# Performance work log

Hardware: AMD Instinct MI355X
Metric: run time of the kernel (lower is better)

The kernel has to match this reference:

```python
import math
import jax, jax.numpy as jnp
import numpy as np

N_GAUSS = 1_000_000
EPS = 1e-8


def setup_inputs() -> dict:
    key = jax.random.key(0)
    k1, k2, k3 = jax.random.split(key, 3)
    init_extent = 50.0
    means = (jax.random.uniform(k1, (N_GAUSS, 3), dtype=jnp.float32) - 0.5) * 2.0 * init_extent
    log_scales = jnp.full((N_GAUSS, 3), math.log(0.05), dtype=jnp.float32)
    quats = jax.random.normal(k2, (N_GAUSS, 4), dtype=jnp.float32)
    sh_coeffs = jax.random.normal(k3, (N_GAUSS, 16, 3), dtype=jnp.float32) * 0.01
    opa_logit = math.log(0.1 / 0.9)  # inverse_sigmoid(init_opacity=0.1)
    opacity_camera = jnp.full((N_GAUSS, 1), opa_logit, dtype=jnp.float32)
    opacity_lidar = jnp.full((N_GAUSS, 1), opa_logit, dtype=jnp.float32)
    camera_to_world = jnp.eye(4, dtype=jnp.float32)
    lidar_to_world = jnp.eye(4, dtype=jnp.float32)
    intrinsics = jnp.array([[1000.0, 0.0, 800.0], [0.0, 1000.0, 450.0], [0.0, 0.0, 1.0]], dtype=jnp.float32)
    return dict(means=means, log_scales=log_scales, quats=quats, sh_coeffs=sh_coeffs,
                opacity_camera=opacity_camera, opacity_lidar=opacity_lidar,
                camera_to_world=camera_to_world, intrinsics=intrinsics,
                lidar_to_world=lidar_to_world,
                rgb_width=1600, rgb_height=900, lidar_width=1024, lidar_height=128,
                fov_min_deg=-25, fov_max_deg=3, near_plane=1, far_plane=100)


def _bilinear_scatter(u, v, w, vals, H, W, wrap_u):
    """Scatter vals [N,C] with weights w [N] at continuous pixel coords (u,v)
    using bilinear splatting. Returns [H, W, C+1] (weighted vals, weight sum)."""
    u0 = jnp.floor(u)
    v0 = jnp.floor(v)
    fu = u - u0
    fv = v - v0
    u0i = u0.astype(jnp.int32)
    v0i = v0.astype(jnp.int32)
    acc = jnp.zeros((H * W, vals.shape[-1] + 1), dtype=vals.dtype)
    corners = ((0, 0, (1.0 - fu) * (1.0 - fv)), (1, 0, fu * (1.0 - fv)),
               (0, 1, (1.0 - fu) * fv), (1, 1, fu * fv))
    for du, dv, cw in corners:
        ui = u0i + du
        vi = v0i + dv
        if wrap_u:
            ui = jnp.mod(ui, W)
            ok_u = jnp.ones_like(ui, dtype=bool)
        else:
            ok_u = (ui >= 0) & (ui < W)
        ok = ok_u & (vi >= 0) & (vi < H)
        ww = w * cw * ok.astype(w.dtype)
        idx = jnp.clip(vi, 0, H - 1) * W + jnp.clip(ui, 0, W - 1)
        payload = jnp.concatenate([vals * ww[:, None], ww[:, None]], axis=-1)
        acc = acc.at[idx].add(payload)
    return acc.reshape(H, W, -1)


def reference(means, log_scales, quats, sh_coeffs, opacity_camera, opacity_lidar,
              camera_to_world, intrinsics, lidar_to_world,
              rgb_width, rgb_height, lidar_width, lidar_height,
              fov_min_deg, fov_max_deg, near_plane, far_plane):
    H, W = int(rgb_height), int(rgb_width)
    HL, WL = int(lidar_height), int(lidar_width)
    near = float(near_plane)
    far = float(far_plane)

    # ---- camera (point-splat proxy of gsplat rasterization) ----
    w2c = jnp.linalg.inv(camera_to_world)
    pts_c = means @ w2c[:3, :3].T + w2c[:3, 3]  # [N,3] camera frame
    x, y, z = pts_c[:, 0], pts_c[:, 1], pts_c[:, 2]
    valid_c = (z > near) & (z < far)
    zs = jnp.where(valid_c, z, 1.0)
    u = intrinsics[0, 0] * x / zs + intrinsics[0, 2]
    v = intrinsics[1, 1] * y / zs + intrinsics[1, 2]
    opa_c = jax.nn.sigmoid(jnp.clip(opacity_camera[:, 0], -20.0, 20.0))
    colors = jax.nn.sigmoid(sh_coeffs[:, 0, :])  # DC band, as in render_rgb
    wc = opa_c * valid_c.astype(opa_c.dtype)
    vals_c = jnp.concatenate([colors, z[:, None]], axis=-1)  # [N,4] (rgb, depth)
    acc = _bilinear_scatter(u, v, wc, vals_c, H, W, wrap_u=False)
    wsum = acc[..., 4]
    alpha = jnp.clip(wsum, 0.0, 1.0)
    rgb = acc[..., :3] / (wsum[..., None] + EPS) * alpha[..., None]  # black background
    depth = acc[..., 3] / (wsum + EPS)

    # ---- LiDAR (custom spherical bilinear range-image splat, mean aggregation) ----
    w2l = jnp.linalg.inv(lidar_to_world)
    pts_l = means @ w2l[:3, :3].T + w2l[:3, 3]
    r = jnp.linalg.norm(pts_l, axis=-1)
    az = jnp.arctan2(pts_l[:, 1], pts_l[:, 0])
    el = jnp.arcsin(pts_l[:, 2] / jnp.maximum(r, 1e-6))
    fmin = math.radians(float(fov_min_deg))
    fmax = math.radians(float(fov_max_deg))
    uL = (az / (2.0 * jnp.pi) + 0.5) * WL          # azimuth wraps around
    vL = (fmax - el) / (fmax - fmin) * (HL - 1)    # elevation row
    valid_l = (r > near) & (r < far) & (el >= fmin) & (el <= fmax)
    opa_l = jax.nn.sigmoid(jnp.clip(opacity_lidar[:, 0], -20.0, 20.0))
    wl = opa_l * valid_l.astype(opa_l.dtype)
    acc_l = _bilinear_scatter(uL, vL, wl, r[:, None], HL, WL, wrap_u=True)
    lw = acc_l[..., 1]
    lidar_depth = acc_l[..., 0] / (lw + EPS)  # 'mean' depth aggregation
    lidar_alpha = jnp.clip(lw, 0.0, 1.0)

    return (rgb, depth, alpha, lidar_depth, lidar_alpha)
```

## Files before the change

### kernel.cpp

```cpp
#include <hip/hip_runtime.h>
#include <math.h>

#define EPSV 1e-8f
#define PI_D 3.14159265358979323846

__device__ float g_mats[32];

__device__ __forceinline__ void invert4x4_reg(const float* __restrict__ m,
                                              float* __restrict__ out) {
    double a00=m[0], a01=m[1], a02=m[2], a03=m[3];
    double a10=m[4], a11=m[5], a12=m[6], a13=m[7];
    double a20=m[8], a21=m[9], a22=m[10],a23=m[11];
    double a30=m[12],a31=m[13],a32=m[14],a33=m[15];

    double b00 = a00*a11 - a01*a10;
    double b01 = a00*a12 - a02*a10;
    double b02 = a00*a13 - a03*a10;
    double b03 = a01*a12 - a02*a11;
    double b04 = a01*a13 - a03*a11;
    double b05 = a02*a13 - a03*a12;
    double b06 = a20*a31 - a21*a30;
    double b07 = a20*a32 - a22*a30;
    double b08 = a20*a33 - a23*a30;
    double b09 = a21*a32 - a22*a31;
    double b10 = a21*a33 - a23*a31;
    double b11 = a22*a33 - a23*a32;

    double det = b00*b11 - b01*b10 + b02*b09 + b03*b08 - b04*b07 + b05*b06;
    double inv = 1.0 / det;

    out[0]  = (float)(( a11*b11 - a12*b10 + a13*b09) * inv);
    out[1]  = (float)((-a01*b11 + a02*b10 - a03*b09) * inv);
    out[2]  = (float)(( a31*b05 - a32*b04 + a33*b03) * inv);
    out[3]  = (float)((-a21*b05 + a22*b04 - a23*b03) * inv);
    out[4]  = (float)((-a10*b11 + a12*b08 - a13*b07) * inv);
    out[5]  = (float)(( a00*b11 - a02*b08 + a03*b07) * inv);
    out[6]  = (float)((-a30*b05 + a32*b02 - a33*b01) * inv);
    out[7]  = (float)(( a20*b05 - a22*b02 + a23*b01) * inv);
    out[8]  = (float)(( a10*b10 - a11*b08 + a13*b06) * inv);
    out[9]  = (float)((-a00*b10 + a01*b08 - a03*b06) * inv);
    out[10] = (float)(( a30*b04 - a31*b02 + a33*b00) * inv);
    out[11] = (float)((-a20*b04 + a21*b02 - a23*b00) * inv);
    out[12] = (float)((-a10*b09 + a11*b07 - a12*b06) * inv);
    out[13] = (float)(( a00*b09 - a01*b07 + a02*b06) * inv);
    out[14] = (float)((-a30*b03 + a31*b01 - a32*b00) * inv);
    out[15] = (float)(( a20*b03 - a21*b01 + a22*b00) * inv);
}

__global__ void prep_kernel(const float* __restrict__ c2w,
                            const float* __restrict__ l2w) {
    if (blockIdx.x == 0 && threadIdx.x == 0) {
        invert4x4_reg(c2w, g_mats);
        invert4x4_reg(l2w, g_mats + 16);
    }
}

__device__ __forceinline__ float sigmoid_clipped(float x) {
    #pragma clang fp contract(off)
    x = fminf(fmaxf(x, -20.0f), 20.0f);
    return 1.0f / (1.0f + expf(-x));
}

template<int MODE>
__global__ __launch_bounds__(256) void scatter_acc(
    const float* __restrict__ means,
    const float* __restrict__ sh,
    const float* __restrict__ opa_c,
    const float* __restrict__ opa_l,
    const float* __restrict__ intr,
    float* __restrict__ acc,
    const int* __restrict__ p_W, const int* __restrict__ p_H,
    const int* __restrict__ p_WL, const int* __restrict__ p_HL,
    const int* __restrict__ p_fmin, const int* __restrict__ p_fmax,
    const int* __restrict__ p_near, const int* __restrict__ p_far,
    int N)
{
    #pragma clang fp contract(off)
    const int T = (N + 1) >> 1;
    const int t = blockIdx.x * blockDim.x + threadIdx.x;
    if (t >= T) return;

    const int W = *p_W, H = *p_H, WL = *p_WL, HL = *p_HL;
    const float nearp = (float)(*p_near);
    const float farp  = (float)(*p_far);
    const double dfmin = (double)(*p_fmin) * PI_D / 180.0;
    const double dfmax = (double)(*p_fmax) * PI_D / 180.0;
    const float ffmin  = (float)dfmin;
    const float ffmax  = (float)dfmax;
    const float denomL = (float)(dfmax - dfmin);
    const float twopi  = (float)(2.0 * PI_D);

    const long long HW = (long long)W * H;

    float* C  = acc;
    float* Wp = (MODE == 4) ? (C + 4 * HW) : nullptr;
    float* L  = C + (MODE == 8 ? 8 : 5) * HW;

    const float fx = intr[0], cx = intr[2], fy = intr[4], cy = intr[5];
    const float* w2c = g_mats;
    const float* w2l = g_mats + 16;

    float mx[2], my[2], mz[2], oc[2], ol[2];
    int   gi[2];
    bool  gv[2];
    #pragma unroll
    for (int k = 0; k < 2; k++) {
        int i = t + k * T;
        gv[k] = (i < N);
        int ii = gv[k] ? i : 0;
        gi[k] = ii;
        mx[k] = means[3 * ii + 0];
        my[k] = means[3 * ii + 1];
        mz[k] = means[3 * ii + 2];
        oc[k] = opa_c[ii];
        ol[k] = opa_l[ii];
    }

    #pragma unroll
    for (int k = 0; k < 2; k++) {
        if (!gv[k]) continue;
        const float px = mx[k], py = my[k], pz = mz[k];

        {
            float x = w2c[0] * px + w2c[1] * py + w2c[2]  * pz + w2c[3];
            float y = w2c[4] * px + w2c[5] * py + w2c[6]  * pz + w2c[7];
            float z = w2c[8] * px + w2c[9] * py + w2c[10] * pz + w2c[11];
            if (z > nearp && z < farp) {
                float u = fx * x / z + cx;
                float v = fy * y / z + cy;
                float wc = sigmoid_clipped(oc[k]);
                const float* shp = sh + 48LL * gi[k];
                float c0 = 1.0f / (1.0f + expf(-shp[0]));
                float c1 = 1.0f / (1.0f + expf(-shp[1]));
                float c2 = 1.0f / (1.0f + expf(-shp[2]));

                float u0f = floorf(u), v0f = floorf(v);
                float fu = u - u0f, fv = v - v0f;
                int u0 = (int)u0f, v0 = (int)v0f;
                #pragma unroll
                for (int c = 0; c < 4; c++) {
                    int du = c & 1, dv = c >> 1;
                    int ui = u0 + du, vi = v0 + dv;
                    if (ui >= 0 && ui < W && vi >= 0 && vi < H) {
                        float cw = (du ? fu : 1.0f - fu) * (dv ? fv : 1.0f - fv);
                        float ww = wc * cw;
                        long long idx = (long long)vi * W + ui;
                        float* g = C + idx * (MODE == 8 ? 8 : 4);
                        atomicAdd(g + 0, c0 * ww);
                        atomicAdd(g + 1, c1 * ww);
                        atomicAdd(g + 2, c2 * ww);
                        atomicAdd(g + 3, z * ww);
                        if (MODE == 8) atomicAdd(g + 4, ww);
                        else           atomicAdd(Wp + idx, ww);
                    }
                }
            }
        }

        {
            float x = w2l[0] * px + w2l[1] * py + w2l[2]  * pz + w2l[3];
            float y = w2l[4] * px + w2l[5] * py + w2l[6]  * pz + w2l[7];
            float z = w2l[8] * px + w2l[9] * py + w2l[10] * pz + w2l[11];
            float rr = ((x * x) + (y * y)) + (z * z);
            float r = sqrtf(rr);
            float q  = z / fmaxf(r, 1e-6f);
            float el = (float)asin((double)q);
            if (r > nearp && r < farp && el >= ffmin && el <= ffmax) {
                float az = (float)atan2((double)y, (double)x);
                float uL = (az / twopi + 0.5f) * (float)WL;
                float vL = (ffmax - el) / denomL * (float)(HL - 1);
                float wl = sigmoid_clipped(ol[k]);

                float u0f = floorf(uL), v0f = floorf(vL);
                float fu = uL - u0f, fv = vL - v0f;
                int u0 = (int)u0f, v0 = (int)v0f;
                #pragma unroll
                for (int c = 0; c < 4; c++) {
                    int du = c & 1, dv = c >> 1;
                    int ui = u0 + du, vi = v0 + dv;
                    if (ui >= WL) ui -= WL;
                    if (vi >= 0 && vi < HL) {
                        float cw = (du ? fu : 1.0f - fu) * (dv ? fv : 1.0f - fv);
                        float ww = wl * cw;
                        long long idx = (long long)vi * WL + ui;
                        atomicAdd(L + 2 * idx + 0, r * ww);
                        atomicAdd(L + 2 * idx + 1, ww);
                    }
                }
            }
        }
    }
}

template<int MODE>
__global__ __launch_bounds__(256) void finalize_acc(
    const float* __restrict__ acc,
    float* __restrict__ out,
    const int* __restrict__ p_W, const int* __restrict__ p_H,
    const int* __restrict__ p_WL, const int* __restrict__ p_HL)
{
    const int W = *p_W, H = *p_H, WL = *p_WL, HL = *p_HL;
    const long long HW = (long long)W * H;
    const long long LHW = (long long)WL * HL;
    const long long depthOff = 3 * HW;
    const long long alphaOff = 4 * HW;
    const long long ldOff    = 5 * HW;
    const long long laOff    = 5 * HW + LHW;

    const float* C  = acc;
    const float* Wp = (MODE == 4) ? (C + 4 * HW) : nullptr;
    const float* L  = C + (MODE == 8 ? 8 : 5) * HW;

    long long i = (long long)blockIdx.x * blockDim.x + threadIdx.x;
    if (i < HW) {
        const float* g = C + i * (MODE == 8 ? 8 : 4);
        float4 p = *reinterpret_cast<const float4*>(g);
        float wsum = (MODE == 8) ? g[4] : Wp[i];
        float a = fminf(fmaxf(wsum, 0.0f), 1.0f);
        float inv = 1.0f / (wsum + EPSV);
        float s = inv * a;
        out[3 * i + 0] = p.x * s;
        out[3 * i + 1] = p.y * s;
        out[3 * i + 2] = p.z * s;
        out[depthOff + i] = p.w * inv;
        out[alphaOff + i] = a;
    }
    if (i < LHW) {
        float2 l = *reinterpret_cast<const float2*>(L + 2 * i);
        out[ldOff + i] = l.x * (1.0f / (l.y + EPSV));
        out[laOff + i] = fminf(fmaxf(l.y, 0.0f), 1.0f);
    }
}

__global__ __launch_bounds__(256) void scatter_fb(
    const float* __restrict__ means,
    const float* __restrict__ sh,
    const float* __restrict__ opa_c,
    const float* __restrict__ opa_l,
    const float* __restrict__ intr,
    const int* __restrict__ p_W, const int* __restrict__ p_H,
    const int* __restrict__ p_WL, const int* __restrict__ p_HL,
    const int* __restrict__ p_fmin, const int* __restrict__ p_fmax,
    const int* __restrict__ p_near, const int* __restrict__ p_far,
    float* __restrict__ out, int N)
{
    #pragma clang fp contract(off)
    const int T = (N + 1) >> 1;
    const int t = blockIdx.x * blockDim.x + threadIdx.x;
    if (t >= T) return;

    const int W = *p_W, H = *p_H, WL = *p_WL, HL = *p_HL;
    const float nearp = (float)(*p_near);
    const float farp  = (float)(*p_far);
    const double dfmin = (double)(*p_fmin) * PI_D / 180.0;
    const double dfmax = (double)(*p_fmax) * PI_D / 180.0;
    const float ffmin  = (float)dfmin;
    const float ffmax  = (float)dfmax;
    const float denomL = (float)(dfmax - dfmin);
    const float twopi  = (float)(2.0 * PI_D);

    const long long HW = (long long)W * H;
    const long long LHW = (long long)WL * HL;
    const long long depthOff = 3 * HW;
    const long long alphaOff = 4 * HW;
    const long long ldOff    = 5 * HW;
    const long long laOff    = 5 * HW + LHW;

    const float fx = intr[0], cx = intr[2], fy = intr[4], cy = intr[5];
    const float* w2c = g_mats;
    const float* w2l = g_mats + 16;

    float mx[2], my[2], mz[2], oc[2], ol[2];
    int   gi[2];
    bool  gv[2];
    #pragma unroll
    for (int k = 0; k < 2; k++) {
        int i = t + k * T;
        gv[k] = (i < N);
        int ii = gv[k] ? i : 0;
        gi[k] = ii;
        mx[k] = means[3 * ii + 0];
        my[k] = means[3 * ii + 1];
        mz[k] = means[3 * ii + 2];
        oc[k] = opa_c[ii];
        ol[k] = opa_l[ii];
    }

    #pragma unroll
    for (int k = 0; k < 2; k++) {
        if (!gv[k]) continue;
        const float px = mx[k], py = my[k], pz = mz[k];
        {
            float x = w2c[0] * px + w2c[1] * py + w2c[2]  * pz + w2c[3];
            float y = w2c[4] * px + w2c[5] * py + w2c[6]  * pz + w2c[7];
            float z = w2c[8] * px + w2c[9] * py + w2c[10] * pz + w2c[11];
            if (z > nearp && z < farp) {
                float u = fx * x / z + cx;
                float v = fy * y / z + cy;
                float wc = sigmoid_clipped(oc[k]);
                const float* shp = sh + 48LL * gi[k];
                float c0 = 1.0f / (1.0f + expf(-shp[0]));
                float c1 = 1.0f / (1.0f + expf(-shp[1]));
                float c2 = 1.0f / (1.0f + expf(-shp[2]));

                float u0f = floorf(u), v0f = floorf(v);
                float fu = u - u0f, fv = v - v0f;
                int u0 = (int)u0f, v0 = (int)v0f;
                #pragma unroll
                for (int c = 0; c < 4; c++) {
                    int du = c & 1, dv = c >> 1;
                    int ui = u0 + du, vi = v0 + dv;
                    if (ui >= 0 && ui < W && vi >= 0 && vi < H) {
                        float cw = (du ? fu : 1.0f - fu) * (dv ? fv : 1.0f - fv);
                        float ww = wc * cw;
                        long long idx = (long long)vi * W + ui;
                        atomicAdd(&out[idx * 3 + 0], c0 * ww);
                        atomicAdd(&out[idx * 3 + 1], c1 * ww);
                        atomicAdd(&out[idx * 3 + 2], c2 * ww);
                        atomicAdd(&out[depthOff + idx], z * ww);
                        atomicAdd(&out[alphaOff + idx], ww);
                    }
                }
            }
        }
        {
            float x = w2l[0] * px + w2l[1] * py + w2l[2]  * pz + w2l[3];
            float y = w2l[4] * px + w2l[5] * py + w2l[6]  * pz + w2l[7];
            float z = w2l[8] * px + w2l[9] * py + w2l[10] * pz + w2l[11];
            float rr = ((x * x) + (y * y)) + (z * z);
            float r = sqrtf(rr);
            float q  = z / fmaxf(r, 1e-6f);
            float el = (float)asin((double)q);
            if (r > nearp && r < farp && el >= ffmin && el <= ffmax) {
                float az = (float)atan2((double)y, (double)x);
                float uL = (az / twopi + 0.5f) * (float)WL;
                float vL = (ffmax - el) / denomL * (float)(HL - 1);
                float wl = sigmoid_clipped(ol[k]);

                float u0f = floorf(uL), v0f = floorf(vL);
                float fu = uL - u0f, fv = vL - v0f;
                int u0 = (int)u0f, v0 = (int)v0f;
                #pragma unroll
                for (int c = 0; c < 4; c++) {
                    int du = c & 1, dv = c >> 1;
                    int ui = u0 + du, vi = v0 + dv;
                    if (ui >= WL) ui -= WL;
                    if (vi >= 0 && vi < HL) {
                        float cw = (du ? fu : 1.0f - fu) * (dv ? fv : 1.0f - fv);
                        float ww = wl * cw;
                        long long idx = (long long)vi * WL + ui;
                        atomicAdd(&out[ldOff + idx], r * ww);
                        atomicAdd(&out[laOff + idx], ww);
                    }
                }
            }
        }
    }
}

__global__ __launch_bounds__(256) void finalize_fb(
    float* __restrict__ out,
    const int* __restrict__ p_W, const int* __restrict__ p_H,
    const int* __restrict__ p_WL, const int* __restrict__ p_HL)
{
    const int W = *p_W, H = *p_H, WL = *p_WL, HL = *p_HL;
    const long long HW = (long long)W * H;
    const long long LHW = (long long)WL * HL;
    const long long depthOff = 3 * HW;
    const long long alphaOff = 4 * HW;
    const long long ldOff    = 5 * HW;
    const long long laOff    = 5 * HW + LHW;

    long long i = (long long)blockIdx.x * blockDim.x + threadIdx.x;
    if (i < HW) {
        float wsum = out[alphaOff + i];
        float a = fminf(fmaxf(wsum, 0.0f), 1.0f);
        float inv = 1.0f / (wsum + EPSV);
        float s = inv * a;
        out[3 * i + 0] *= s;
        out[3 * i + 1] *= s;
        out[3 * i + 2] *= s;
        out[depthOff + i] *= inv;
        out[alphaOff + i] = a;
    }
    if (i < LHW) {
        float wsum = out[laOff + i];
        out[ldOff + i] *= 1.0f / (wsum + EPSV);
        out[laOff + i] = fminf(fmaxf(wsum, 0.0f), 1.0f);
    }
}

extern "C" void kernel_launch(void* const* d_in, const int* in_sizes, int n_in,
                              void* d_out, int out_size, void* d_ws, size_t ws_size,
                              hipStream_t stream) {
    const float* means  = (const float*)d_in[0];
    const float* sh     = (const float*)d_in[3];
    const float* opa_c  = (const float*)d_in[4];
    const float* opa_l  = (const float*)d_in[5];
    const float* c2w    = (const float*)d_in[6];
    const float* intr   = (const float*)d_in[7];
    const float* l2w    = (const float*)d_in[8];
    const int* p_W    = (const int*)d_in[9];
    const int* p_H    = (const int*)d_in[10];
    const int* p_WL   = (const int*)d_in[11];
    const int* p_HL   = (const int*)d_in[12];
    const int* p_fmin = (const int*)d_in[13];
    const int* p_fmax = (const int*)d_in[14];
    const int* p_near = (const int*)d_in[15];
    const int* p_far  = (const int*)d_in[16];

    const int N = in_sizes[0] / 3;
    float* out = (float*)d_out;
    float* acc = (float*)d_ws;

    const long long HW  = 1600LL * 900LL;
    const long long LHW = 1024LL * 128LL;
    const size_t bytes8 = (8 * (size_t)HW + 2 * (size_t)LHW) * sizeof(float);
    const size_t bytes4 = (5 * (size_t)HW + 2 * (size_t)LHW) * sizeof(float);

    const int T = (N + 1) / 2;
    const int sgrid = (T + 255) / 256;
    const int fgrid = (int)((HW + 255) / 256);

    prep_kernel<<<1, 64, 0, stream>>>(c2w, l2w);

    if (ws_size >= bytes8) {
        hipMemsetAsync(d_ws, 0, bytes8, stream);
        scatter_acc<8><<<sgrid, 256, 0, stream>>>(
            means, sh, opa_c, opa_l, intr, acc,
            p_W, p_H, p_WL, p_HL, p_fmin, p_fmax, p_near, p_far, N);
        finalize_acc<8><<<fgrid, 256, 0, stream>>>(
            acc, out, p_W, p_H, p_WL, p_HL);
    } else if (ws_size >= bytes4) {
        hipMemsetAsync(d_ws, 0, bytes4, stream);
        scatter_acc<4><<<sgrid, 256, 0, stream>>>(
            means, sh, opa_c, opa_l, intr, acc,
            p_W, p_H, p_WL, p_HL, p_fmin, p_fmax, p_near, p_far, N);
        finalize_acc<4><<<fgrid, 256, 0, stream>>>(
            acc, out, p_W, p_H, p_WL, p_HL);
    } else {
        hipMemsetAsync(d_out, 0, (size_t)out_size * sizeof(float), stream);
        scatter_fb<<<sgrid, 256, 0, stream>>>(
            means, sh, opa_c, opa_l, intr,
            p_W, p_H, p_WL, p_HL, p_fmin, p_fmax, p_near, p_far,
            out, N);
        finalize_fb<<<fgrid, 256, 0, stream>>>(
            out, p_W, p_H, p_WL, p_HL);
    }
}
```

Measured before the change: 434.2 us.

## Split camera and lidar scatter kernels and replicate lidar accumulators to cut contention

```diff
diff --git a/kernel.cpp b/kernel.cpp
--- a/kernel.cpp
+++ b/kernel.cpp
@@ -3,6 +3,7 @@
 
 #define EPSV 1e-8f
 #define PI_D 3.14159265358979323846
+#define NREP 8
 
 __device__ float g_mats[32];
 
@@ -61,13 +62,72 @@
     return 1.0f / (1.0f + expf(-x));
 }
 
-template<int MODE>
-__global__ __launch_bounds__(256) void scatter_acc(
+__global__ __launch_bounds__(256) void scatter_cam(
     const float* __restrict__ means,
     const float* __restrict__ sh,
     const float* __restrict__ opa_c,
+    const float* __restrict__ intr,
+    float* __restrict__ acc,
+    const int* __restrict__ p_W, const int* __restrict__ p_H,
+    const int* __restrict__ p_near, const int* __restrict__ p_far,
+    int N)
+{
+    #pragma clang fp contract(off)
+    const int t = blockIdx.x * blockDim.x + threadIdx.x;
+    if (t >= N) return;
+
+    const int W = *p_W, H = *p_H;
+    const float nearp = (float)(*p_near);
+    const float farp  = (float)(*p_far);
+    const long long HW = (long long)W * H;
+
+    float* C  = acc;
+    float* Wp = acc + 4 * HW;
+
+    const float fx = intr[0], cx = intr[2], fy = intr[4], cy = intr[5];
+    const float* w2c = g_mats;
+
+    const float px = means[3 * t + 0];
+    const float py = means[3 * t + 1];
+    const float pz = means[3 * t + 2];
+
+    float x = w2c[0] * px + w2c[1] * py + w2c[2]  * pz + w2c[3];
+    float y = w2c[4] * px + w2c[5] * py + w2c[6]  * pz + w2c[7];
+    float z = w2c[8] * px + w2c[9] * py + w2c[10] * pz + w2c[11];
+    if (!(z > nearp && z < farp)) return;
+
+    float u = fx * x / z + cx;
+    float v = fy * y / z + cy;
+    float wc = sigmoid_clipped(opa_c[t]);
+    const float* shp = sh + 48LL * t;
+    float c0 = 1.0f / (1.0f + expf(-shp[0]));
+    float c1 = 1.0f / (1.0f + expf(-shp[1]));
+    float c2 = 1.0f / (1.0f + expf(-shp[2]));
+
+    float u0f = floorf(u), v0f = floorf(v);
+    float fu = u - u0f, fv = v - v0f;
+    int u0 = (int)u0f, v0 = (int)v0f;
+    #pragma unroll
+    for (int c = 0; c < 4; c++) {
+        int du = c & 1, dv = c >> 1;
+        int ui = u0 + du, vi = v0 + dv;
+        if (ui >= 0 && ui < W && vi >= 0 && vi < H) {
+            float cw = (du ? fu : 1.0f - fu) * (dv ? fv : 1.0f - fv);
+            float ww = wc * cw;
+            long long idx = (long long)vi * W + ui;
+            float* g = C + idx * 4;
+            atomicAdd(g + 0, c0 * ww);
+            atomicAdd(g + 1, c1 * ww);
+            atomicAdd(g + 2, c2 * ww);
+            atomicAdd(g + 3, z * ww);
+            atomicAdd(Wp + idx, ww);
+        }
+    }
+}
+
+__global__ __launch_bounds__(256) void scatter_lid(
+    const float* __restrict__ means,
     const float* __restrict__ opa_l,
-    const float* __restrict__ intr,
     float* __restrict__ acc,
     const int* __restrict__ p_W, const int* __restrict__ p_H,
     const int* __restrict__ p_WL, const int* __restrict__ p_HL,
@@ -76,9 +136,8 @@
     int N)
 {
     #pragma clang fp contract(off)
-    const int T = (N + 1) >> 1;
     const int t = blockIdx.x * blockDim.x + threadIdx.x;
-    if (t >= T) return;
+    if (t >= N) return;
 
     const int W = *p_W, H = *p_H, WL = *p_WL, HL = *p_HL;
     const float nearp = (float)(*p_near);
@@ -90,109 +149,49 @@
     const float denomL = (float)(dfmax - dfmin);
     const float twopi  = (float)(2.0 * PI_D);
 
-    const long long HW = (long long)W * H;
-
-    float* C  = acc;
-    float* Wp = (MODE == 4) ? (C + 4 * HW) : nullptr;
-    float* L  = C + (MODE == 8 ? 8 : 5) * HW;
-
-    const float fx = intr[0], cx = intr[2], fy = intr[4], cy = intr[5];
-    const float* w2c = g_mats;
+    const long long HW  = (long long)W * H;
+    const long long LHW = (long long)WL * HL;
+
+    float* Lr = acc + 5 * HW + (long long)(blockIdx.x & (NREP - 1)) * 2 * LHW;
+
     const float* w2l = g_mats + 16;
 
-    float mx[2], my[2], mz[2], oc[2], ol[2];
-    int   gi[2];
-    bool  gv[2];
+    const float px = means[3 * t + 0];
+    const float py = means[3 * t + 1];
+    const float pz = means[3 * t + 2];
+
+    float x = w2l[0] * px + w2l[1] * py + w2l[2]  * pz + w2l[3];
+    float y = w2l[4] * px + w2l[5] * py + w2l[6]  * pz + w2l[7];
+    float z = w2l[8] * px + w2l[9] * py + w2l[10] * pz + w2l[11];
+    float rr = ((x * x) + (y * y)) + (z * z);
+    float r = sqrtf(rr);
+    float q  = z / fmaxf(r, 1e-6f);
+    float el = (float)asin((double)q);
+    if (!(r > nearp && r < farp && el >= ffmin && el <= ffmax)) return;
+
+    float az = (float)atan2((double)y, (double)x);
+    float uL = (az / twopi + 0.5f) * (float)WL;
+    float vL = (ffmax - el) / denomL * (float)(HL - 1);
+    float wl = sigmoid_clipped(opa_l[t]);
+
+    float u0f = floorf(uL), v0f = floorf(vL);
+    float fu = uL - u0f, fv = vL - v0f;
+    int u0 = (int)u0f, v0 = (int)v0f;
     #pragma unroll
-    for (int k = 0; k < 2; k++) {
-        int i = t + k * T;
-        gv[k] = (i < N);
-        int ii = gv[k] ? i : 0;
-        gi[k] = ii;
-        mx[k] = means[3 * ii + 0];
-        my[k] = means[3 * ii + 1];
-        mz[k] = means[3 * ii + 2];
-        oc[k] = opa_c[ii];
-        ol[k] = opa_l[ii];
-    }
-
-    #pragma unroll
-    for (int k = 0; k < 2; k++) {
-        if (!gv[k]) continue;
-        const float px = mx[k], py = my[k], pz = mz[k];
-
-        {
-            float x = w2c[0] * px + w2c[1] * py + w2c[2]  * pz + w2c[3];
-            float y = w2c[4] * px + w2c[5] * py + w2c[6]  * pz + w2c[7];
-            float z = w2c[8] * px + w2c[9] * py + w2c[10] * pz + w2c[11];
-            if (z > nearp && z < farp) {
-                float u = fx * x / z + cx;
-                float v = fy * y / z + cy;
-                float wc = sigmoid_clipped(oc[k]);
-                const float* shp = sh + 48LL * gi[k];
-                float c0 = 1.0f / (1.0f + expf(-shp[0]));
-                float c1 = 1.0f / (1.0f + expf(-shp[1]));
-                float c2 = 1.0f / (1.0f + expf(-shp[2]));
-
-                float u0f = floorf(u), v0f = floorf(v);
-                float fu = u - u0f, fv = v - v0f;
-                int u0 = (int)u0f, v0 = (int)v0f;
-                #pragma unroll
-                for (int c = 0; c < 4; c++) {
-                    int du = c & 1, dv = c >> 1;
-                    int ui = u0 + du, vi = v0 + dv;
-                    if (ui >= 0 && ui < W && vi >= 0 && vi < H) {
-                        float cw = (du ? fu : 1.0f - fu) * (dv ? fv : 1.0f - fv);
-                        float ww = wc * cw;
-                        long long idx = (long long)vi * W + ui;
-                        float* g = C + idx * (MODE == 8 ? 8 : 4);
-                        atomicAdd(g + 0, c0 * ww);
-                        atomicAdd(g + 1, c1 * ww);
-                        atomicAdd(g + 2, c2 * ww);
-                        atomicAdd(g + 3, z * ww);
-                        if (MODE == 8) atomicAdd(g + 4, ww);
-                        else           atomicAdd(Wp + idx, ww);
-                    }
-                }
-            }
+    for (int c = 0; c < 4; c++) {
+        int du = c & 1, dv = c >> 1;
+        int ui = u0 + du, vi = v0 + dv;
+        if (ui >= WL) ui -= WL;
+        if (vi >= 0 && vi < HL) {
+            float cw = (du ? fu : 1.0f - fu) * (dv ? fv : 1.0f - fv);
+            float ww = wl * cw;
+            long long idx = (long long)vi * WL + ui;
+            atomicAdd(Lr + 2 * idx + 0, r * ww);
+            atomicAdd(Lr + 2 * idx + 1, ww);
         }
-
-        {
-            float x = w2l[0] * px + w2l[1] * py + w2l[2]  * pz + w2l[3];
-            float y = w2l[4] * px + w2l[5] * py + w2l[6]  * pz + w2l[7];
-            float z = w2l[8] * px + w2l[9] * py + w2l[10] * pz + w2l[11];
-            float rr = ((x * x) + (y * y)) + (z * z);
-            float r = sqrtf(rr);
-            float q  = z / fmaxf(r, 1e-6f);
-            float el = (float)asin((double)q);
-            if (r > nearp && r < farp && el >= ffmin && el <= ffmax) {
-                float az = (float)atan2((double)y, (double)x);
-                float uL = (az / twopi + 0.5f) * (float)WL;
-                float vL = (ffmax - el) / denomL * (float)(HL - 1);
-                float wl = sigmoid_clipped(ol[k]);
-
-                float u0f = floorf(uL), v0f = floorf(vL);
-                float fu = uL - u0f, fv = vL - v0f;
-                int u0 = (int)u0f, v0 = (int)v0f;
-                #pragma unroll
-                for (int c = 0; c < 4; c++) {
-                    int du = c & 1, dv = c >> 1;
-                    int ui = u0 + du, vi = v0 + dv;
-                    if (ui >= WL) ui -= WL;
-                    if (vi >= 0 && vi < HL) {
-                        float cw = (du ? fu : 1.0f - fu) * (dv ? fv : 1.0f - fv);
-                        float ww = wl * cw;
-                        long long idx = (long long)vi * WL + ui;
-                        atomicAdd(L + 2 * idx + 0, r * ww);
-                        atomicAdd(L + 2 * idx + 1, ww);
-                    }
-                }
-            }
-        }
-    }
-}
-
-template<int MODE>
+    }
+}
+
 __global__ __launch_bounds__(256) void finalize_acc(
     const float* __restrict__ acc,
     float* __restrict__ out,
@@ -208,14 +207,13 @@
     const long long laOff    = 5 * HW + LHW;
 
     const float* C  = acc;
-    const float* Wp = (MODE == 4) ? (C + 4 * HW) : nullptr;
-    const float* L  = C + (MODE == 8 ? 8 : 5) * HW;
+    const float* Wp = acc + 4 * HW;
+    const float* L  = acc + 5 * HW;
 
     long long i = (long long)blockIdx.x * blockDim.x + threadIdx.x;
     if (i < HW) {
-        const float* g = C + i * (MODE == 8 ? 8 : 4);
-        float4 p = *reinterpret_cast<const float4*>(g);
-        float wsum = (MODE == 8) ? g[4] : Wp[i];
+        float4 p = *reinterpret_cast<const float4*>(C + 4 * i);
+        float wsum = Wp[i];
         float a = fminf(fmaxf(wsum, 0.0f), 1.0f);
         float inv = 1.0f / (wsum + EPSV);
         float s = inv * a;
@@ -226,9 +224,15 @@
         out[alphaOff + i] = a;
     }
     if (i < LHW) {
-        float2 l = *reinterpret_cast<const float2*>(L + 2 * i);
-        out[ldOff + i] = l.x * (1.0f / (l.y + EPSV));
-        out[laOff + i] = fminf(fmaxf(l.y, 0.0f), 1.0f);
+        float ld = 0.0f, lw = 0.0f;
+        #pragma unroll
+        for (int k = 0; k < NREP; k++) {
+            float2 l = *reinterpret_cast<const float2*>(L + (long long)k * 2 * LHW + 2 * i);
+            ld += l.x;
+            lw += l.y;
+        }
+        out[ldOff + i] = ld * (1.0f / (lw + EPSV));
+        out[laOff + i] = fminf(fmaxf(lw, 0.0f), 1.0f);
     }
 }
 
@@ -245,9 +249,8 @@
     float* __restrict__ out, int N)
 {
     #pragma clang fp contract(off)
-    const int T = (N + 1) >> 1;
     const int t = blockIdx.x * blockDim.x + threadIdx.x;
-    if (t >= T) return;
+    if (t >= N) return;
 
     const int W = *p_W, H = *p_H, WL = *p_WL, HL = *p_HL;
     const float nearp = (float)(*p_near);
@@ -270,88 +273,70 @@
     const float* w2c = g_mats;
     const float* w2l = g_mats + 16;
 
-    float mx[2], my[2], mz[2], oc[2], ol[2];
-    int   gi[2];
-    bool  gv[2];
-    #pragma unroll
-    for (int k = 0; k < 2; k++) {
-        int i = t + k * T;
-        gv[k] = (i < N);
-        int ii = gv[k] ? i : 0;
-        gi[k] = ii;
-        mx[k] = means[3 * ii + 0];
-        my[k] = means[3 * ii + 1];
-        mz[k] = means[3 * ii + 2];
-        oc[k] = opa_c[ii];
-        ol[k] = opa_l[ii];
-    }
-
-    #pragma unroll
-    for (int k = 0; k < 2; k++) {
-        if (!gv[k]) continue;
-        const float px = mx[k], py = my[k], pz = mz[k];
-        {
-            float x = w2c[0] * px + w2c[1] * py + w2c[2]  * pz + w2c[3];
-            float y = w2c[4] * px + w2c[5] * py + w2c[6]  * pz + w2c[7];
-            float z = w2c[8] * px + w2c[9] * py + w2c[10] * pz + w2c[11];
-            if (z > nearp && z < farp) {
-                float u = fx * x / z + cx;
-                float v = fy * y / z + cy;
-                float wc = sigmoid_clipped(oc[k]);
-                const float* shp = sh + 48LL * gi[k];
-                float c0 = 1.0f / (1.0f + expf(-shp[0]));
-                float c1 = 1.0f / (1.0f + expf(-shp[1]));
-                float c2 = 1.0f / (1.0f + expf(-shp[2]));
-
-                float u0f = floorf(u), v0f = floorf(v);
-                float fu = u - u0f, fv = v - v0f;
-                int u0 = (int)u0f, v0 = (int)v0f;
-                #pragma unroll
-                for (int c = 0; c < 4; c++) {
-                    int du = c & 1, dv = c >> 1;
-                    int ui = u0 + du, vi = v0 + dv;
-                    if (ui >= 0 && ui < W && vi >= 0 && vi < H) {
-                        float cw = (du ? fu : 1.0f - fu) * (dv ? fv : 1.0f - fv);
-                        float ww = wc * cw;
-                        long long idx = (long long)vi * W + ui;
-                        atomicAdd(&out[idx * 3 + 0], c0 * ww);
-                        atomicAdd(&out[idx * 3 + 1], c1 * ww);
-                        atomicAdd(&out[idx * 3 + 2], c2 * ww);
-                        atomicAdd(&out[depthOff + idx], z * ww);
-                        atomicAdd(&out[alphaOff + idx], ww);
-                    }
+    const float px = means[3 * t + 0];
+    const float py = means[3 * t + 1];
+    const float pz = means[3 * t + 2];
+    {
+        float x = w2c[0] * px + w2c[1] * py + w2c[2]  * pz + w2c[3];
+        float y = w2c[4] * px + w2c[5] * py + w2c[6]  * pz + w2c[7];
+        float z = w2c[8] * px + w2c[9] * py + w2c[10] * pz + w2c[11];
+        if (z > nearp && z < farp) {
+            float u = fx * x / z + cx;
+            float v = fy * y / z + cy;
+            float wc = sigmoid_clipped(opa_c[t]);
+            const float* shp = sh + 48LL * t;
+            float c0 = 1.0f / (1.0f + expf(-shp[0]));
+            float c1 = 1.0f / (1.0f + expf(-shp[1]));
+            float c2 = 1.0f / (1.0f + expf(-shp[2]));
+
+            float u0f = floorf(u), v0f = floorf(v);
+            float fu = u - u0f, fv = v - v0f;
+            int u0 = (int)u0f, v0 = (int)v0f;
+            #pragma unroll
+            for (int c = 0; c < 4; c++) {
+                int du = c & 1, dv = c >> 1;
+                int ui = u0 + du, vi = v0 + dv;
+                if (ui >= 0 && ui < W && vi >= 0 && vi < H) {
+                    float cw = (du ? fu : 1.0f - fu) * (dv ? fv : 1.0f - fv);
+                    float ww = wc * cw;
+                    long long idx = (long long)vi * W + ui;
+                    atomicAdd(&out[idx * 3 + 0], c0 * ww);
+                    atomicAdd(&out[idx * 3 + 1], c1 * ww);
+                    atomicAdd(&out[idx * 3 + 2], c2 * ww);
+                    atomicAdd(&out[depthOff + idx], z * ww);
+                    atomicAdd(&out[alphaOff + idx], ww);
                 }
             }
         }
-        {
-            float x = w2l[0] * px + w2l[1] * py + w2l[2]  * pz + w2l[3];
-            float y = w2l[4] * px + w2l[5] * py + w2l[6]  * pz + w2l[7];
-            float z = w2l[8] * px + w2l[9] * py + w2l[10] * pz + w2l[11];
-            float rr = ((x * x) + (y * y)) + (z * z);
-            float r = sqrtf(rr);
-            float q  = z / fmaxf(r, 1e-6f);
-            float el = (float)asin((double)q);
-            if (r > nearp && r < farp && el >= ffmin && el <= ffmax) {
-                float az = (float)atan2((double)y, (double)x);
-                float uL = (az / twopi + 0.5f) * (float)WL;
-                float vL = (ffmax - el) / denomL * (float)(HL - 1);
-                float wl = sigmoid_clipped(ol[k]);
-
-                float u0f = floorf(uL), v0f = floorf(vL);
-                float fu = uL - u0f, fv = vL - v0f;
-                int u0 = (int)u0f, v0 = (int)v0f;
-                #pragma unroll
-                for (int c = 0; c < 4; c++) {
-                    int du = c & 1, dv = c >> 1;
-                    int ui = u0 + du, vi = v0 + dv;
-                    if (ui >= WL) ui -= WL;
-                    if (vi >= 0 && vi < HL) {
-                        float cw = (du ? fu : 1.0f - fu) * (dv ? fv : 1.0f - fv);
-                        float ww = wl * cw;
-                        long long idx = (long long)vi * WL + ui;
-                        atomicAdd(&out[ldOff + idx], r * ww);
-                        atomicAdd(&out[laOff + idx], ww);
-                    }
+    }
+    {
+        float x = w2l[0] * px + w2l[1] * py + w2l[2]  * pz + w2l[3];
+        float y = w2l[4] * px + w2l[5] * py + w2l[6]  * pz + w2l[7];
+        float z = w2l[8] * px + w2l[9] * py + w2l[10] * pz + w2l[11];
+        float rr = ((x * x) + (y * y)) + (z * z);
+        float r = sqrtf(rr);
+        float q  = z / fmaxf(r, 1e-6f);
+        float el = (float)asin((double)q);
+        if (r > nearp && r < farp && el >= ffmin && el <= ffmax) {
+            float az = (float)atan2((double)y, (double)x);
+            float uL = (az / twopi + 0.5f) * (float)WL;
+            float vL = (ffmax - el) / denomL * (float)(HL - 1);
+            float wl = sigmoid_clipped(opa_l[t]);
+
+            float u0f = floorf(uL), v0f = floorf(vL);
+            float fu = uL - u0f, fv = vL - v0f;
+            int u0 = (int)u0f, v0 = (int)v0f;
+            #pragma unroll
+            for (int c = 0; c < 4; c++) {
+                int du = c & 1, dv = c >> 1;
+                int ui = u0 + du, vi = v0 + dv;
+                if (ui >= WL) ui -= WL;
+                if (vi >= 0 && vi < HL) {
+                    float cw = (du ? fu : 1.0f - fu) * (dv ? fv : 1.0f - fv);
+                    float ww = wl * cw;
+                    long long idx = (long long)vi * WL + ui;
+                    atomicAdd(&out[ldOff + idx], r * ww);
+                    atomicAdd(&out[laOff + idx], ww);
                 }
             }
         }
@@ -415,28 +400,23 @@
 
     const long long HW  = 1600LL * 900LL;
     const long long LHW = 1024LL * 128LL;
-    const size_t bytes8 = (8 * (size_t)HW + 2 * (size_t)LHW) * sizeof(float);
-    const size_t bytes4 = (5 * (size_t)HW + 2 * (size_t)LHW) * sizeof(float);
-
-    const int T = (N + 1) / 2;
-    const int sgrid = (T + 255) / 256;
+    const size_t need_bytes =
+        (5 * (size_t)HW + (size_t)NREP * 2 * (size_t)LHW) * sizeof(float);
+
+    const int sgrid = (N + 255) / 256;
     const int fgrid = (int)((HW + 255) / 256);
 
     prep_kernel<<<1, 64, 0, stream>>>(c2w, l2w);
 
-    if (ws_size >= bytes8) {
-        hipMemsetAsync(d_ws, 0, bytes8, stream);
-        scatter_acc<8><<<sgrid, 256, 0, stream>>>(
-            means, sh, opa_c, opa_l, intr, acc,
+    if (ws_size >= need_bytes) {
+        hipMemsetAsync(d_ws, 0, need_bytes, stream);
+        scatter_cam<<<sgrid, 256, 0, stream>>>(
+            means, sh, opa_c, intr, acc,
+            p_W, p_H, p_near, p_far, N);
+        scatter_lid<<<sgrid, 256, 0, stream>>>(
+            means, opa_l, acc,
             p_W, p_H, p_WL, p_HL, p_fmin, p_fmax, p_near, p_far, N);
-        finalize_acc<8><<<fgrid, 256, 0, stream>>>(
-            acc, out, p_W, p_H, p_WL, p_HL);
-    } else if (ws_size >= bytes4) {
-        hipMemsetAsync(d_ws, 0, bytes4, stream);
-        scatter_acc<4><<<sgrid, 256, 0, stream>>>(
-            means, sh, opa_c, opa_l, intr, acc,
-            p_W, p_H, p_WL, p_HL, p_fmin, p_fmax, p_near, p_far, N);
-        finalize_acc<4><<<fgrid, 256, 0, stream>>>(
+        finalize_acc<<<fgrid, 256, 0, stream>>>(
             acc, out, p_W, p_H, p_WL, p_HL);
     } else {
         hipMemsetAsync(d_out, 0, (size_t)out_size * sizeof(float), stream);
```

Result: no change. 426.3 us (-1.8%).
